# Optimization experiments

Hardware: AMD Instinct MI355X
Metric: run time of the kernel (lower is better)

The kernel has to match this reference:

```python
import jax, jax.numpy as jnp
import numpy as np

GROUP_SIZE = 128  # per-group absmax scaling along the feature dim
ALPHA = 1.0       # group_size > 0 branch forces alpha = 1.0
# 4-bit signed non-uniform 'flint' grid (e2m1-style), sorted ascending, 15 levels
GRID_VALUES = np.array([-6.0, -4.0, -3.0, -2.0, -1.5, -1.0, -0.5, 0.0,
                        0.5, 1.0, 1.5, 2.0, 3.0, 4.0, 6.0], dtype=np.float32)


def quantize_with_grid(x, grid, group_size, alpha):
    """Group-wise fake quantization: scale each group by alpha*absmax/max|grid|,
    snap to nearest grid value, dequantize. Matches ANT quantize_with_grid."""
    orig_shape = x.shape
    xg = x.reshape(-1, group_size)                       # [G, group_size]
    gmax = jnp.max(jnp.abs(grid))
    maxv = jnp.max(jnp.abs(xg), axis=1, keepdims=True) * alpha
    scale = maxv / gmax                                  # [G, 1]
    scale = jnp.where(scale == 0, jnp.float32(1.0), scale)
    xs = xg / scale
    # nearest-grid lookup via midpoints + searchsorted (memory-light, exact)
    mid = (grid[1:] + grid[:-1]) * 0.5                   # [K-1]
    idx = jnp.searchsorted(mid, xs)                      # [G, group_size]
    q = jnp.take(grid, idx)
    return (q * scale).reshape(orig_shape)


def setup_inputs() -> dict:
    key = jax.random.key(0)
    k1, k2, k3 = jax.random.split(key, 3)
    x = jax.random.normal(k1, (4, 4096, 4096), dtype=jnp.float32)
    # weight buffer is the already-dequantized (calibrated) weight
    weight = jax.random.normal(k2, (1024, 4096), dtype=jnp.float32) * 0.02
    bias = jax.random.normal(k3, (1024,), dtype=jnp.float32) * 0.01
    grid = jnp.asarray(GRID_VALUES)
    return {"x": x, "weight": weight, "bias": bias, "grid": grid}


def reference(x, weight, bias, grid):
    # ANT_Linear.forward, calibrated steady state:
    #   input_2d = x.reshape(-1, in_features)
    #   deq_input = quantize_with_grid(input_2d, grid, group_size, alpha=1.0)
    #   out = F.linear(deq_input, weight) + bias
    out_shape = x.shape[:-1] + (weight.shape[0],)
    x2d = x.reshape(-1, x.shape[-1])                     # [N, in_features]
    deq = quantize_with_grid(x2d, grid, GROUP_SIZE, ALPHA)
    out = jnp.einsum('ni,oi->no', deq, weight) + bias    # [N, out_features]
    return out.reshape(out_shape)
```

## Files before the change

### kernel.cpp

```cpp
#include <hip/hip_runtime.h>
#include <hip/hip_bf16.h>

using bf16x8 = __attribute__((ext_vector_type(8))) __bf16;
using f32x4  = __attribute__((ext_vector_type(4))) float;
typedef unsigned short ushort_t;

#define M_DIM 16384
#define K_DIM 4096
#define N_DIM 1024

#define BARR() __builtin_amdgcn_s_barrier()

__device__ __forceinline__ unsigned short f2bf(float f) {
  __hip_bfloat16 h = __float2bfloat16(f);
  return *reinterpret_cast<unsigned short*>(&h);
}

__device__ __forceinline__ float snap(float a) {
  float q = 0.0f;
  q += (a > 0.25f) ? 0.5f : 0.0f;
  q += (a > 0.75f) ? 0.5f : 0.0f;
  q += (a > 1.25f) ? 0.5f : 0.0f;
  q += (a > 1.75f) ? 0.5f : 0.0f;
  q += (a > 2.5f)  ? 1.0f : 0.0f;
  q += (a > 3.5f)  ? 1.0f : 0.0f;
  q += (a > 5.0f)  ? 2.0f : 0.0f;
  return q;
}

__device__ __forceinline__ unsigned short qdq(float xv, float rs, float scale) {
  float xs = xv * rs;
  float q  = copysignf(snap(fabsf(xs)), xs);
  return f2bf(q * scale);
}

__global__ __launch_bounds__(256) void quant_kernel(const float* __restrict__ x,
                                                    unsigned short* __restrict__ dq) {
  const int wid = (blockIdx.x << 2) + (threadIdx.x >> 6);
  const int l   = threadIdx.x & 63;
  const int sub = l >> 4, t = l & 15;
  const size_t base = ((size_t)wid * 4 + sub) * 128;
  const float4* px = reinterpret_cast<const float4*>(x + base);
  float4 v0 = px[t];
  float4 v1 = px[16 + t];
  float amax = fmaxf(fmaxf(fmaxf(fabsf(v0.x), fabsf(v0.y)), fmaxf(fabsf(v0.z), fabsf(v0.w))),
                     fmaxf(fmaxf(fabsf(v1.x), fabsf(v1.y)), fmaxf(fabsf(v1.z), fabsf(v1.w))));
  #pragma unroll
  for (int m = 1; m < 16; m <<= 1) amax = fmaxf(amax, __shfl_xor(amax, m, 64));
  float scale = amax / 6.0f;
  if (scale == 0.0f) scale = 1.0f;
  const float rs = 1.0f / scale;
  ushort4 o0, o1;
  o0.x = qdq(v0.x, rs, scale); o0.y = qdq(v0.y, rs, scale);
  o0.z = qdq(v0.z, rs, scale); o0.w = qdq(v0.w, rs, scale);
  o1.x = qdq(v1.x, rs, scale); o1.y = qdq(v1.y, rs, scale);
  o1.z = qdq(v1.z, rs, scale); o1.w = qdq(v1.w, rs, scale);
  reinterpret_cast<ushort4*>(dq + base)[t]      = o0;
  reinterpret_cast<ushort4*>(dq + base)[16 + t] = o1;
}

__global__ __launch_bounds__(256) void wconv_kernel(const float* __restrict__ w,
                                                    unsigned short* __restrict__ o) {
  const int n4 = (N_DIM * K_DIM) / 4;
  for (int i = blockIdx.x * 256 + threadIdx.x; i < n4; i += gridDim.x * 256) {
    float4 v = reinterpret_cast<const float4*>(w)[i];
    ushort4 u;
    u.x = f2bf(v.x); u.y = f2bf(v.y); u.z = f2bf(v.z); u.w = f2bf(v.w);
    reinterpret_cast<ushort4*>(o)[i] = u;
  }
}

__device__ __forceinline__ bf16x8 lds_ld(const ushort_t* p) {
  return *reinterpret_cast<const bf16x8*>(p);
}

__device__ __forceinline__ void stg(const ushort_t* g0, const ushort_t* g1,
                                    ushort_t (&slot)[8192], int wid) {
  __builtin_amdgcn_global_load_lds((const __attribute__((address_space(1))) void*)g0,
      (__attribute__((address_space(3))) void*)(&slot[wid * 512]), 16, 0, 0);
  __builtin_amdgcn_global_load_lds((const __attribute__((address_space(1))) void*)g1,
      (__attribute__((address_space(3))) void*)(&slot[4096 + wid * 512]), 16, 0, 0);
}

template<bool S12, bool S34, int VM>
__device__ __forceinline__ void tile_iter(
    int t,
    ushort_t (&rA)[8192],  ushort_t (&rB)[8192],
    ushort_t (&dB1)[8192], ushort_t (&dA1)[8192],
    ushort_t (&dB0)[8192], ushort_t (&dA0)[8192],
    int wid, const int (&roA)[8], const int (&roB)[4], int swz0, int swz1,
    const ushort_t* pa0, const ushort_t* pa1,
    const ushort_t* pb0, const ushort_t* pb1,
    f32x4 (&acc)[8][4]) {
  bf16x8 aL0[4], aL1[4], aH0[4], aH1[4], b0[4], b1[4];

  #pragma unroll
  for (int i = 0; i < 4; ++i) {
    aL0[i] = lds_ld(&rA[roA[i] + swz0]);
    aL1[i] = lds_ld(&rA[roA[i] + swz1]);
  }
  #pragma unroll
  for (int n = 0; n < 2; ++n) {
    b0[n] = lds_ld(&rB[roB[n] + swz0]);
    b1[n] = lds_ld(&rB[roB[n] + swz1]);
  }

  #pragma unroll
  for (int n = 2; n < 4; ++n) {
    b0[n] = lds_ld(&rB[roB[n] + swz0]);
    b1[n] = lds_ld(&rB[roB[n] + swz1]);
  }
  if constexpr (S12)
    stg(pb0 + (size_t)128 * K_DIM + (size_t)(t + 1) * 64,
        pb1 + (size_t)128 * K_DIM + (size_t)(t + 1) * 64, dB1, wid);
  __builtin_amdgcn_s_setprio(1);
  #pragma unroll
  for (int i = 0; i < 4; ++i)
    #pragma unroll
    for (int n = 0; n < 2; ++n) {
      acc[i][n] = __builtin_amdgcn_mfma_f32_16x16x32_bf16(aL0[i], b0[n], acc[i][n], 0, 0, 0);
      acc[i][n] = __builtin_amdgcn_mfma_f32_16x16x32_bf16(aL1[i], b1[n], acc[i][n], 0, 0, 0);
    }
  __builtin_amdgcn_s_setprio(0);
  BARR();

  #pragma unroll
  for (int i = 0; i < 4; ++i) {
    aH0[i] = lds_ld(&rA[roA[4 + i] + swz0]);
    aH1[i] = lds_ld(&rA[roA[4 + i] + swz1]);
  }
  if constexpr (S12)
    stg(pa0 + (size_t)128 * K_DIM + (size_t)(t + 1) * 64,
        pa1 + (size_t)128 * K_DIM + (size_t)(t + 1) * 64, dA1, wid);
  __builtin_amdgcn_s_setprio(1);
  #pragma unroll
  for (int i = 0; i < 4; ++i)
    #pragma unroll
    for (int n = 2; n < 4; ++n) {
      acc[i][n] = __builtin_amdgcn_mfma_f32_16x16x32_bf16(aL0[i], b0[n], acc[i][n], 0, 0, 0);
      acc[i][n] = __builtin_amdgcn_mfma_f32_16x16x32_bf16(aL1[i], b1[n], acc[i][n], 0, 0, 0);
    }
  __builtin_amdgcn_s_setprio(0);
  BARR();

  if constexpr (S34)
    stg(pb0 + (size_t)(t + 2) * 64, pb1 + (size_t)(t + 2) * 64, dB0, wid);
  __builtin_amdgcn_s_setprio(1);
  #pragma unroll
  for (int i = 0; i < 4; ++i)
    #pragma unroll
    for (int n = 2; n < 4; ++n) {
      acc[4 + i][n] = __builtin_amdgcn_mfma_f32_16x16x32_bf16(aH0[i], b0[n], acc[4 + i][n], 0, 0, 0);
      acc[4 + i][n] = __builtin_amdgcn_mfma_f32_16x16x32_bf16(aH1[i], b1[n], acc[4 + i][n], 0, 0, 0);
    }
  __builtin_amdgcn_s_setprio(0);
  BARR();

  if constexpr (S34)
    stg(pa0 + (size_t)(t + 2) * 64, pa1 + (size_t)(t + 2) * 64, dA0, wid);
  __builtin_amdgcn_s_setprio(1);
  #pragma unroll
  for (int i = 0; i < 4; ++i)
    #pragma unroll
    for (int n = 0; n < 2; ++n) {
      acc[4 + i][n] = __builtin_amdgcn_mfma_f32_16x16x32_bf16(aH0[i], b0[n], acc[4 + i][n], 0, 0, 0);
      acc[4 + i][n] = __builtin_amdgcn_mfma_f32_16x16x32_bf16(aH1[i], b1[n], acc[4 + i][n], 0, 0, 0);
    }
  __builtin_amdgcn_s_setprio(0);
  if constexpr (VM == 4) {
    asm volatile("s_waitcnt vmcnt(4)");
    __builtin_amdgcn_sched_barrier(0);
  } else if constexpr (VM == 0) {
    asm volatile("s_waitcnt vmcnt(0)");
    __builtin_amdgcn_sched_barrier(0);
  }
  BARR();
}

template<int WM, int WH>
__device__ __forceinline__ void krun(
    ushort_t (&sA0p0)[8192], ushort_t (&sA0p1)[8192],
    ushort_t (&sA1p0)[8192], ushort_t (&sA1p1)[8192],
    ushort_t (&sB0p0)[8192], ushort_t (&sB0p1)[8192],
    ushort_t (&sB1p0)[8192], ushort_t (&sB1p1)[8192],
    int wid, const int (&roA)[8], const int (&roB)[4], int swz0, int swz1,
    const ushort_t* pa0, const ushort_t* pa1,
    const ushort_t* pb0, const ushort_t* pb1,
    f32x4 (&acc)[8][4]) {
  ushort_t (&rAp0)[8192] = WM ? sA1p0 : sA0p0;
  ushort_t (&rAp1)[8192] = WM ? sA1p1 : sA0p1;
  ushort_t (&rBp0)[8192] = WH ? sB1p0 : sB0p0;
  ushort_t (&rBp1)[8192] = WH ? sB1p1 : sB0p1;

  stg(pb0, pb1, sB0p0, wid);
  stg(pa0, pa1, sA0p0, wid);
  stg(pb0 + (size_t)128 * K_DIM, pb1 + (size_t)128 * K_DIM, sB1p0, wid);
  stg(pa0 + (size_t)128 * K_DIM, pa1 + (size_t)128 * K_DIM, sA1p0, wid);
  stg(pb0 + 64, pb1 + 64, sB0p1, wid);
  stg(pa0 + 64, pa1 + 64, sA0p1, wid);
  asm volatile("s_waitcnt vmcnt(4)");
  __builtin_amdgcn_sched_barrier(0);
  BARR();

  for (int t = 0; t < 62; t += 2) {
    tile_iter<true, true, 4>(t,     rAp0, rBp0, sB1p1, sA1p1, sB0p0, sA0p0,
                             wid, roA, roB, swz0, swz1, pa0, pa1, pb0, pb1, acc);
    tile_iter<true, true, 4>(t + 1, rAp1, rBp1, sB1p0, sA1p0, sB0p1, sA0p1,
                             wid, roA, roB, swz0, swz1, pa0, pa1, pb0, pb1, acc);
  }
  tile_iter<true, false, 0>(62, rAp0, rBp0, sB1p1, sA1p1, sB0p0, sA0p0,
                            wid, roA, roB, swz0, swz1, pa0, pa1, pb0, pb1, acc);
  tile_iter<false, false, -1>(63, rAp1, rBp1, sB1p0, sA1p0, sB0p1, sA0p1,
                              wid, roA, roB, swz0, swz1, pa0, pa1, pb0, pb1, acc);
}

__global__ __launch_bounds__(512, 2) void gemm256(const ushort_t* __restrict__ A,
                                                  const ushort_t* __restrict__ B,
                                                  const float* __restrict__ bias,
                                                  float* __restrict__ C) {
  __shared__ ushort_t sA0p0[8192], sA0p1[8192], sA1p0[8192], sA1p1[8192];
  __shared__ ushort_t sB0p0[8192], sB0p1[8192], sB1p0[8192], sB1p1[8192];
  const int tid  = threadIdx.x;
  const int wid  = tid >> 6, lane = tid & 63;
  const int r    = lane & 15, h = lane >> 4;
  const int wm   = wid >> 2, wn = wid & 3;
  const int bn   = blockIdx.x, bm = blockIdx.y;

  const int x7   = lane & 7;
  const int swz0 = ((h) ^ x7) << 3;
  const int swz1 = ((4 | h) ^ x7) << 3;
  int roA[8], roB[4];
  #pragma unroll
  for (int m = 0; m < 8; ++m) roA[m] = (m * 16 + r) * 64;
  #pragma unroll
  for (int n = 0; n < 4; ++n) roB[n] = ((wn & 1) * 64 + n * 16 + r) * 64;

  const int srow0 = tid >> 3;
  const int cst   = ((tid & 7) ^ (srow0 & 7)) << 3;
  const ushort_t* pa0 = A + (size_t)(bm * 256 + srow0) * K_DIM + cst;
  const ushort_t* pa1 = A + (size_t)(bm * 256 + 64 + srow0) * K_DIM + cst;
  const ushort_t* pb0 = B + (size_t)(bn * 256 + srow0) * K_DIM + cst;
  const ushort_t* pb1 = B + (size_t)(bn * 256 + 64 + srow0) * K_DIM + cst;

  f32x4 acc[8][4];
  #pragma unroll
  for (int m = 0; m < 8; ++m)
    #pragma unroll
    for (int n = 0; n < 4; ++n) acc[m][n] = (f32x4){0.f, 0.f, 0.f, 0.f};

  const int wh = wn >> 1;
  if (wm == 0) {
    if (wh == 0) krun<0, 0>(sA0p0, sA0p1, sA1p0, sA1p1, sB0p0, sB0p1, sB1p0, sB1p1,
                            wid, roA, roB, swz0, swz1, pa0, pa1, pb0, pb1, acc);
    else         krun<0, 1>(sA0p0, sA0p1, sA1p0, sA1p1, sB0p0, sB0p1, sB1p0, sB1p1,
                            wid, roA, roB, swz0, swz1, pa0, pa1, pb0, pb1, acc);
  } else {
    if (wh == 0) krun<1, 0>(sA0p0, sA0p1, sA1p0, sA1p1, sB0p0, sB0p1, sB1p0, sB1p1,
                            wid, roA, roB, swz0, swz1, pa0, pa1, pb0, pb1, acc);
    else         krun<1, 1>(sA0p0, sA0p1, sA1p0, sA1p1, sB0p0, sB0p1, sB1p0, sB1p1,
                            wid, roA, roB, swz0, swz1, pa0, pa1, pb0, pb1, acc);
  }

  const int orow = bm * 256 + wm * 128;
  const int ocol = bn * 256 + wn * 64;
  #pragma unroll
  for (int n = 0; n < 4; ++n) {
    const int col = ocol + n * 16 + r;
    const float bv = bias[col];
    #pragma unroll
    for (int m = 0; m < 8; ++m) {
      const int rb = orow + m * 16 + h * 4;
      #pragma unroll
      for (int j = 0; j < 4; ++j)
        C[(size_t)(rb + j) * N_DIM + col] = acc[m][n][j] + bv;
    }
  }
}

__global__ __launch_bounds__(256) void fused_naive(const float* __restrict__ x,
                                                   const float* __restrict__ w,
                                                   const float* __restrict__ bias,
                                                   float* __restrict__ out) {
  __shared__ float xq[K_DIM];
  const int row = blockIdx.x;
  const float* xr = x + (size_t)row * K_DIM;
  const int t = threadIdx.x;
  const int g = t >> 3, s = t & 7;
  float vals[16];
  float amax = 0.f;
  #pragma unroll
  for (int i = 0; i < 16; ++i) {
    vals[i] = xr[g * 128 + s * 16 + i];
    amax = fmaxf(amax, fabsf(vals[i]));
  }
  #pragma unroll
  for (int m = 1; m < 8; m <<= 1) amax = fmaxf(amax, __shfl_xor(amax, m, 64));
  float scale = amax / 6.0f;
  if (scale == 0.f) scale = 1.f;
  const float rs = 1.0f / scale;
  #pragma unroll
  for (int i = 0; i < 16; ++i) {
    float xs = vals[i] * rs;
    xq[g * 128 + s * 16 + i] = copysignf(snap(fabsf(xs)), xs) * scale;
  }
  __syncthreads();
  #pragma unroll
  for (int i = 0; i < 4; ++i) {
    const int o = i * 256 + t;
    const float* wrow = w + (size_t)o * K_DIM;
    float acc = 0.f;
    for (int k = 0; k < K_DIM; k += 4) {
      float4 wv = *reinterpret_cast<const float4*>(wrow + k);
      acc += xq[k] * wv.x + xq[k + 1] * wv.y + xq[k + 2] * wv.z + xq[k + 3] * wv.w;
    }
    out[(size_t)row * N_DIM + o] = acc + bias[o];
  }
}

extern "C" void kernel_launch(void* const* d_in, const int* in_sizes, int n_in,
                              void* d_out, int out_size, void* d_ws, size_t ws_size,
                              hipStream_t stream) {
  const float* x    = (const float*)d_in[0];
  const float* wgt  = (const float*)d_in[1];
  const float* bias = (const float*)d_in[2];
  float* out = (float*)d_out;

  const size_t deq_bytes = (size_t)M_DIM * K_DIM * 2;
  const size_t wb_bytes  = (size_t)N_DIM * K_DIM * 2;
  if (ws_size >= deq_bytes + wb_bytes) {
    ushort_t* deq = (ushort_t*)d_ws;
    ushort_t* wb  = (ushort_t*)((char*)d_ws + deq_bytes);
    quant_kernel<<<(M_DIM * (K_DIM / 128)) / 16, 256, 0, stream>>>(x, deq);
    wconv_kernel<<<1024, 256, 0, stream>>>(wgt, wb);
    gemm256<<<dim3(N_DIM / 256, M_DIM / 256), 512, 0, stream>>>(deq, wb, bias, out);
  } else {
    fused_naive<<<M_DIM, 256, 0, stream>>>(x, wgt, bias, out);
  }
}
```

Measured before the change: 223.4 us.

## Replace direct global-to-LDS loads with register-staged prefetch pipeline

The GEMM main loop no longer uses global_load_lds to copy tiles straight into shared memory. It issues global_load_dwordx4 into registers one stage ahead and writes them to LDS later in the tile iteration, with hand-placed vmcnt and lgkmcnt waits. The aim is to decouple global latency from the LDS write path and control the schedule more tightly. The cost is extra VGPRs for the staged data and explicit ds_write instructions, which could hurt occupancy at 512 threads with 2 blocks per CU.

```diff
diff --git a/kernel.cpp b/kernel.cpp
--- a/kernel.cpp
+++ b/kernel.cpp
@@ -1,8 +1,9 @@
 #include <hip/hip_runtime.h>
 #include <hip/hip_bf16.h>
 
-using bf16x8 = __attribute__((ext_vector_type(8))) __bf16;
-using f32x4  = __attribute__((ext_vector_type(4))) float;
+using bf16x8  = __attribute__((ext_vector_type(8))) __bf16;
+using f32x4   = __attribute__((ext_vector_type(4))) float;
+using ushortx8 = __attribute__((ext_vector_type(8))) unsigned short;
 typedef unsigned short ushort_t;
 
 #define M_DIM 16384
@@ -10,6 +11,7 @@
 #define N_DIM 1024
 
 #define BARR() __builtin_amdgcn_s_barrier()
+#define GLOAD(q, p) asm volatile("global_load_dwordx4 %0, %1, off" : "=v"(q) : "v"(p))
 
 __device__ __forceinline__ unsigned short f2bf(float f) {
   __hip_bfloat16 h = __float2bfloat16(f);
@@ -74,23 +76,26 @@
   return *reinterpret_cast<const bf16x8*>(p);
 }
 
-__device__ __forceinline__ void stg(const ushort_t* g0, const ushort_t* g1,
-                                    ushort_t (&slot)[8192], int wid) {
-  __builtin_amdgcn_global_load_lds((const __attribute__((address_space(1))) void*)g0,
-      (__attribute__((address_space(3))) void*)(&slot[wid * 512]), 16, 0, 0);
-  __builtin_amdgcn_global_load_lds((const __attribute__((address_space(1))) void*)g1,
-      (__attribute__((address_space(3))) void*)(&slot[4096 + wid * 512]), 16, 0, 0);
-}
-
-template<bool S12, bool S34, int VM>
+__device__ __forceinline__ void pstage(ushort_t (&slot)[8192], const ushort_t* g0,
+                                       const ushort_t* g1, int dsw) {
+  ushortx8 q0 = *reinterpret_cast<const ushortx8*>(g0);
+  ushortx8 q1 = *reinterpret_cast<const ushortx8*>(g1);
+  *reinterpret_cast<ushortx8*>(&slot[dsw])        = q0;
+  *reinterpret_cast<ushortx8*>(&slot[4096 + dsw]) = q1;
+}
+
+template<bool W12, bool L12, bool W34, bool L34>
 __device__ __forceinline__ void tile_iter(
     int t,
     ushort_t (&rA)[8192],  ushort_t (&rB)[8192],
     ushort_t (&dB1)[8192], ushort_t (&dA1)[8192],
     ushort_t (&dB0)[8192], ushort_t (&dA0)[8192],
-    int wid, const int (&roA)[8], const int (&roB)[4], int swz0, int swz1,
+    int dsw,
+    const int (&roA)[8], const int (&roB)[4], int swz0, int swz1,
     const ushort_t* pa0, const ushort_t* pa1,
     const ushort_t* pb0, const ushort_t* pb1,
+    ushortx8 (&gBa)[2], ushortx8 (&gBb)[2],
+    ushortx8 (&gAa)[2], ushortx8 (&gAb)[2],
     f32x4 (&acc)[8][4]) {
   bf16x8 aL0[4], aL1[4], aH0[4], aH1[4], b0[4], b1[4];
 
@@ -105,14 +110,20 @@
     b1[n] = lds_ld(&rB[roB[n] + swz1]);
   }
 
+  if constexpr (W12) {
+    asm volatile("s_waitcnt vmcnt(2)" ::: "memory");
+    *reinterpret_cast<ushortx8*>(&dB1[dsw])        = gBa[0];
+    *reinterpret_cast<ushortx8*>(&dB1[4096 + dsw]) = gBa[1];
+  }
+  if constexpr (L12) {
+    GLOAD(gBb[0], pb0 + (size_t)(t + 2) * 64);
+    GLOAD(gBb[1], pb1 + (size_t)(t + 2) * 64);
+  }
   #pragma unroll
   for (int n = 2; n < 4; ++n) {
     b0[n] = lds_ld(&rB[roB[n] + swz0]);
     b1[n] = lds_ld(&rB[roB[n] + swz1]);
   }
-  if constexpr (S12)
-    stg(pb0 + (size_t)128 * K_DIM + (size_t)(t + 1) * 64,
-        pb1 + (size_t)128 * K_DIM + (size_t)(t + 1) * 64, dB1, wid);
   __builtin_amdgcn_s_setprio(1);
   #pragma unroll
   for (int i = 0; i < 4; ++i)
@@ -122,16 +133,23 @@
       acc[i][n] = __builtin_amdgcn_mfma_f32_16x16x32_bf16(aL1[i], b1[n], acc[i][n], 0, 0, 0);
     }
   __builtin_amdgcn_s_setprio(0);
-  BARR();
-
+  if constexpr (W12) asm volatile("s_waitcnt lgkmcnt(0)" ::: "memory");
+  BARR();
+
+  if constexpr (W12) {
+    asm volatile("s_waitcnt vmcnt(%0)" :: "i"(W34 ? 2 : 0) : "memory");
+    *reinterpret_cast<ushortx8*>(&dA1[dsw])        = gAa[0];
+    *reinterpret_cast<ushortx8*>(&dA1[4096 + dsw]) = gAa[1];
+  }
+  if constexpr (L12) {
+    GLOAD(gAb[0], pa0 + (size_t)(t + 2) * 64);
+    GLOAD(gAb[1], pa1 + (size_t)(t + 2) * 64);
+  }
   #pragma unroll
   for (int i = 0; i < 4; ++i) {
     aH0[i] = lds_ld(&rA[roA[4 + i] + swz0]);
     aH1[i] = lds_ld(&rA[roA[4 + i] + swz1]);
   }
-  if constexpr (S12)
-    stg(pa0 + (size_t)128 * K_DIM + (size_t)(t + 1) * 64,
-        pa1 + (size_t)128 * K_DIM + (size_t)(t + 1) * 64, dA1, wid);
   __builtin_amdgcn_s_setprio(1);
   #pragma unroll
   for (int i = 0; i < 4; ++i)
@@ -141,10 +159,18 @@
       acc[i][n] = __builtin_amdgcn_mfma_f32_16x16x32_bf16(aL1[i], b1[n], acc[i][n], 0, 0, 0);
     }
   __builtin_amdgcn_s_setprio(0);
-  BARR();
-
-  if constexpr (S34)
-    stg(pb0 + (size_t)(t + 2) * 64, pb1 + (size_t)(t + 2) * 64, dB0, wid);
+  if constexpr (W12) asm volatile("s_waitcnt lgkmcnt(0)" ::: "memory");
+  BARR();
+
+  if constexpr (W34) {
+    asm volatile("s_waitcnt vmcnt(2)" ::: "memory");
+    *reinterpret_cast<ushortx8*>(&dB0[dsw])        = gBb[0];
+    *reinterpret_cast<ushortx8*>(&dB0[4096 + dsw]) = gBb[1];
+  }
+  if constexpr (L34) {
+    GLOAD(gBa[0], pb0 + (size_t)128 * K_DIM + (size_t)(t + 2) * 64);
+    GLOAD(gBa[1], pb1 + (size_t)128 * K_DIM + (size_t)(t + 2) * 64);
+  }
   __builtin_amdgcn_s_setprio(1);
   #pragma unroll
   for (int i = 0; i < 4; ++i)
@@ -154,10 +180,18 @@
       acc[4 + i][n] = __builtin_amdgcn_mfma_f32_16x16x32_bf16(aH1[i], b1[n], acc[4 + i][n], 0, 0, 0);
     }
   __builtin_amdgcn_s_setprio(0);
-  BARR();
-
-  if constexpr (S34)
-    stg(pa0 + (size_t)(t + 2) * 64, pa1 + (size_t)(t + 2) * 64, dA0, wid);
+  if constexpr (W34) asm volatile("s_waitcnt lgkmcnt(0)" ::: "memory");
+  BARR();
+
+  if constexpr (W34) {
+    asm volatile("s_waitcnt vmcnt(2)" ::: "memory");
+    *reinterpret_cast<ushortx8*>(&dA0[dsw])        = gAb[0];
+    *reinterpret_cast<ushortx8*>(&dA0[4096 + dsw]) = gAb[1];
+  }
+  if constexpr (L34) {
+    GLOAD(gAa[0], pa0 + (size_t)128 * K_DIM + (size_t)(t + 2) * 64);
+    GLOAD(gAa[1], pa1 + (size_t)128 * K_DIM + (size_t)(t + 2) * 64);
+  }
   __builtin_amdgcn_s_setprio(1);
   #pragma unroll
   for (int i = 0; i < 4; ++i)
@@ -167,13 +201,7 @@
       acc[4 + i][n] = __builtin_amdgcn_mfma_f32_16x16x32_bf16(aH1[i], b1[n], acc[4 + i][n], 0, 0, 0);
     }
   __builtin_amdgcn_s_setprio(0);
-  if constexpr (VM == 4) {
-    asm volatile("s_waitcnt vmcnt(4)");
-    __builtin_amdgcn_sched_barrier(0);
-  } else if constexpr (VM == 0) {
-    asm volatile("s_waitcnt vmcnt(0)");
-    __builtin_amdgcn_sched_barrier(0);
-  }
+  if constexpr (W34) asm volatile("s_waitcnt lgkmcnt(0)" ::: "memory");
   BARR();
 }
 
@@ -183,7 +211,7 @@
     ushort_t (&sA1p0)[8192], ushort_t (&sA1p1)[8192],
     ushort_t (&sB0p0)[8192], ushort_t (&sB0p1)[8192],
     ushort_t (&sB1p0)[8192], ushort_t (&sB1p1)[8192],
-    int wid, const int (&roA)[8], const int (&roB)[4], int swz0, int swz1,
+    int dsw, const int (&roA)[8], const int (&roB)[4], int swz0, int swz1,
     const ushort_t* pa0, const ushort_t* pa1,
     const ushort_t* pb0, const ushort_t* pb1,
     f32x4 (&acc)[8][4]) {
@@ -192,26 +220,32 @@
   ushort_t (&rBp0)[8192] = WH ? sB1p0 : sB0p0;
   ushort_t (&rBp1)[8192] = WH ? sB1p1 : sB0p1;
 
-  stg(pb0, pb1, sB0p0, wid);
-  stg(pa0, pa1, sA0p0, wid);
-  stg(pb0 + (size_t)128 * K_DIM, pb1 + (size_t)128 * K_DIM, sB1p0, wid);
-  stg(pa0 + (size_t)128 * K_DIM, pa1 + (size_t)128 * K_DIM, sA1p0, wid);
-  stg(pb0 + 64, pb1 + 64, sB0p1, wid);
-  stg(pa0 + 64, pa1 + 64, sA0p1, wid);
-  asm volatile("s_waitcnt vmcnt(4)");
-  __builtin_amdgcn_sched_barrier(0);
+  ushortx8 gBa[2], gBb[2], gAa[2], gAb[2];
+
+  pstage(sB0p0, pb0, pb1, dsw);
+  pstage(sA0p0, pa0, pa1, dsw);
+  pstage(sB1p0, pb0 + (size_t)128 * K_DIM, pb1 + (size_t)128 * K_DIM, dsw);
+  pstage(sA1p0, pa0 + (size_t)128 * K_DIM, pa1 + (size_t)128 * K_DIM, dsw);
+  pstage(sB0p1, pb0 + 64, pb1 + 64, dsw);
+  pstage(sA0p1, pa0 + 64, pa1 + 64, dsw);
+  asm volatile("s_waitcnt vmcnt(0)" ::: "memory");
+  GLOAD(gBa[0], pb0 + (size_t)128 * K_DIM + 64);
+  GLOAD(gBa[1], pb1 + (size_t)128 * K_DIM + 64);
+  GLOAD(gAa[0], pa0 + (size_t)128 * K_DIM + 64);
+  GLOAD(gAa[1], pa1 + (size_t)128 * K_DIM + 64);
+  asm volatile("s_waitcnt lgkmcnt(0)" ::: "memory");
   BARR();
 
   for (int t = 0; t < 62; t += 2) {
-    tile_iter<true, true, 4>(t,     rAp0, rBp0, sB1p1, sA1p1, sB0p0, sA0p0,
-                             wid, roA, roB, swz0, swz1, pa0, pa1, pb0, pb1, acc);
-    tile_iter<true, true, 4>(t + 1, rAp1, rBp1, sB1p0, sA1p0, sB0p1, sA0p1,
-                             wid, roA, roB, swz0, swz1, pa0, pa1, pb0, pb1, acc);
-  }
-  tile_iter<true, false, 0>(62, rAp0, rBp0, sB1p1, sA1p1, sB0p0, sA0p0,
-                            wid, roA, roB, swz0, swz1, pa0, pa1, pb0, pb1, acc);
-  tile_iter<false, false, -1>(63, rAp1, rBp1, sB1p0, sA1p0, sB0p1, sA0p1,
-                              wid, roA, roB, swz0, swz1, pa0, pa1, pb0, pb1, acc);
+    tile_iter<true, true, true, true>(t,     rAp0, rBp0, sB1p1, sA1p1, sB0p0, sA0p0,
+        dsw, roA, roB, swz0, swz1, pa0, pa1, pb0, pb1, gBa, gBb, gAa, gAb, acc);
+    tile_iter<true, true, true, true>(t + 1, rAp1, rBp1, sB1p0, sA1p0, sB0p1, sA0p1,
+        dsw, roA, roB, swz0, swz1, pa0, pa1, pb0, pb1, gBa, gBb, gAa, gAb, acc);
+  }
+  tile_iter<true, false, false, false>(62, rAp0, rBp0, sB1p1, sA1p1, sB0p0, sA0p0,
+      dsw, roA, roB, swz0, swz1, pa0, pa1, pb0, pb1, gBa, gBb, gAa, gAb, acc);
+  tile_iter<false, false, false, false>(63, rAp1, rBp1, sB1p0, sA1p0, sB0p1, sA0p1,
+      dsw, roA, roB, swz0, swz1, pa0, pa1, pb0, pb1, gBa, gBb, gAa, gAb, acc);
 }
 
 __global__ __launch_bounds__(512, 2) void gemm256(const ushort_t* __restrict__ A,
@@ -237,6 +271,7 @@
 
   const int srow0 = tid >> 3;
   const int cst   = ((tid & 7) ^ (srow0 & 7)) << 3;
+  const int dsw   = tid * 8;
   const ushort_t* pa0 = A + (size_t)(bm * 256 + srow0) * K_DIM + cst;
   const ushort_t* pa1 = A + (size_t)(bm * 256 + 64 + srow0) * K_DIM + cst;
   const ushort_t* pb0 = B + (size_t)(bn * 256 + srow0) * K_DIM + cst;
@@ -251,14 +286,14 @@
   const int wh = wn >> 1;
   if (wm == 0) {
     if (wh == 0) krun<0, 0>(sA0p0, sA0p1, sA1p0, sA1p1, sB0p0, sB0p1, sB1p0, sB1p1,
-                            wid, roA, roB, swz0, swz1, pa0, pa1, pb0, pb1, acc);
+                            dsw, roA, roB, swz0, swz1, pa0, pa1, pb0, pb1, acc);
     else         krun<0, 1>(sA0p0, sA0p1, sA1p0, sA1p1, sB0p0, sB0p1, sB1p0, sB1p1,
-                            wid, roA, roB, swz0, swz1, pa0, pa1, pb0, pb1, acc);
+                            dsw, roA, roB, swz0, swz1, pa0, pa1, pb0, pb1, acc);
   } else {
     if (wh == 0) krun<1, 0>(sA0p0, sA0p1, sA1p0, sA1p1, sB0p0, sB0p1, sB1p0, sB1p1,
-                            wid, roA, roB, swz0, swz1, pa0, pa1, pb0, pb1, acc);
+                            dsw, roA, roB, swz0, swz1, pa0, pa1, pb0, pb1, acc);
     else         krun<1, 1>(sA0p0, sA0p1, sA1p0, sA1p1, sB0p0, sB0p1, sB1p0, sB1p1,
-                            wid, roA, roB, swz0, swz1, pa0, pa1, pb0, pb1, acc);
+                            dsw, roA, roB, swz0, swz1, pa0, pa1, pb0, pb1, acc);
   }
 
   const int orow = bm * 256 + wm * 128;
```

After: 342.9 us. 53.5% more time.
